# Kernel optimization log

Measured on AMD Instinct MI355X. Metric: run time of the kernel, lower is better.

## Reference

```python
import jax, jax.numpy as jnp
import numpy as np

T, B, L, D = 4, 2, 2048, 4096

def setup_inputs() -> dict:
    key = jax.random.key(0)
    x = jax.random.normal(key, (T, B, L, D), dtype=jnp.float32)
    return {"x": x}

def reference(x):
    # X_t = sum_{s<=t} x_s ; Y_t = silu(X_t) ; out_t = Y_t - Y_{t-1}, Y_{-1}=0
    X = jnp.cumsum(x, axis=0)            # (T,B,L,D)
    Y = jax.nn.silu(X)                   # act_fn default "silu"
    Y_prev = jnp.concatenate([jnp.zeros_like(Y[:1]), Y[:-1]], axis=0)
    return Y - Y_prev
```

## Files before the change

### kernel.cpp

```cpp
#include <hip/hip_runtime.h>
#include <math.h>


#define T_STEPS 4

__global__ __launch_bounds__(256) void ActSWL_kernel(const float* __restrict__ x,
                                                     float* __restrict__ out,
                                                     long long n_inner_vec,
                                                     long long stride_vec) {
    long long i = (long long)blockIdx.x * blockDim.x + threadIdx.x;
    if (i >= n_inner_vec) return;

    const float4* __restrict__ xv = reinterpret_cast<const float4*>(x);
    float4* __restrict__ ov       = reinterpret_cast<float4*>(out);

    float4 X     = make_float4(0.f, 0.f, 0.f, 0.f);
    float4 Yprev = make_float4(0.f, 0.f, 0.f, 0.f);

#pragma unroll
    for (int t = 0; t < T_STEPS; ++t) {
        float4 v = xv[i + (long long)t * stride_vec];

        X.x += v.x; X.y += v.y; X.z += v.z; X.w += v.w;

        float4 Y;
        Y.x = X.x / (1.0f + __expf(-X.x));
        Y.y = X.y / (1.0f + __expf(-X.y));
        Y.z = X.z / (1.0f + __expf(-X.z));
        Y.w = X.w / (1.0f + __expf(-X.w));

        float4 o;
        o.x = Y.x - Yprev.x;
        o.y = Y.y - Yprev.y;
        o.z = Y.z - Yprev.z;
        o.w = Y.w - Yprev.w;

        ov[i + (long long)t * stride_vec] = o;

        Yprev = Y;
    }
}

extern "C" void kernel_launch(void* const* d_in, const int* in_sizes, int n_in,
                              void* d_out, int out_size, void* d_ws, size_t ws_size,
                              hipStream_t stream) {
    const float* x = (const float*)d_in[0];
    float* out     = (float*)d_out;

    const long long n_total   = (long long)in_sizes[0];
    const long long n_inner   = n_total / T_STEPS;
    const long long n_vec     = n_inner / 4;
    const long long stridev   = n_vec;

    const int block = 256;
    const long long grid = (n_vec + block - 1) / block;

    ActSWL_kernel<<<dim3((unsigned)grid), dim3(block), 0, stream>>>(x, out, n_vec, stridev);
}
```

Measured before the change: 435.8 us.

## Use nontemporal vector loads/stores, hoist loads, fast reciprocal, 32-bit indexing

Rewrites the elementwise cumsum-silu-diff kernel so that all four time-step loads are issued up front as nontemporal loads, and outputs are written with nontemporal stores. The division is replaced with a hardware reciprocal builtin, and index math is switched from 64-bit to 32-bit. The aim is more memory-level parallelism, less cache pollution on a streaming, bandwidth-bound kernel, and cheaper address arithmetic. It trades some precision from the approximate reciprocal and relies on the 32-bit indices staying within range for this size.

```diff
diff --git a/kernel.cpp b/kernel.cpp
--- a/kernel.cpp
+++ b/kernel.cpp
@@ -4,56 +4,54 @@
 
 #define T_STEPS 4
 
-__global__ __launch_bounds__(256) void ActSWL_kernel(const float* __restrict__ x,
-                                                     float* __restrict__ out,
-                                                     long long n_inner_vec,
-                                                     long long stride_vec) {
-    long long i = (long long)blockIdx.x * blockDim.x + threadIdx.x;
-    if (i >= n_inner_vec) return;
+typedef float v4f __attribute__((ext_vector_type(4)));
 
-    const float4* __restrict__ xv = reinterpret_cast<const float4*>(x);
-    float4* __restrict__ ov       = reinterpret_cast<float4*>(out);
+__device__ __forceinline__ v4f silu4(v4f X) {
+    v4f r;
+    r.x = X.x * __builtin_amdgcn_rcpf(1.0f + __expf(-X.x));
+    r.y = X.y * __builtin_amdgcn_rcpf(1.0f + __expf(-X.y));
+    r.z = X.z * __builtin_amdgcn_rcpf(1.0f + __expf(-X.z));
+    r.w = X.w * __builtin_amdgcn_rcpf(1.0f + __expf(-X.w));
+    return r;
+}
 
-    float4 X     = make_float4(0.f, 0.f, 0.f, 0.f);
-    float4 Yprev = make_float4(0.f, 0.f, 0.f, 0.f);
+__global__ __launch_bounds__(256) void ActSWL_kernel(const v4f* __restrict__ xv,
+                                                     v4f* __restrict__ ov,
+                                                     unsigned n_vec) {
+    unsigned i = blockIdx.x * 256u + threadIdx.x;
+    if (i >= n_vec) return;
 
-#pragma unroll
-    for (int t = 0; t < T_STEPS; ++t) {
-        float4 v = xv[i + (long long)t * stride_vec];
+    v4f v0 = __builtin_nontemporal_load(xv + i);
+    v4f v1 = __builtin_nontemporal_load(xv + i + n_vec);
+    v4f v2 = __builtin_nontemporal_load(xv + i + 2u * n_vec);
+    v4f v3 = __builtin_nontemporal_load(xv + i + 3u * n_vec);
 
-        X.x += v.x; X.y += v.y; X.z += v.z; X.w += v.w;
+    v4f X  = v0;
+    v4f y0 = silu4(X);
+    X += v1;
+    v4f y1 = silu4(X);
+    X += v2;
+    v4f y2 = silu4(X);
+    X += v3;
+    v4f y3 = silu4(X);
 
-        float4 Y;
-        Y.x = X.x / (1.0f + __expf(-X.x));
-        Y.y = X.y / (1.0f + __expf(-X.y));
-        Y.z = X.z / (1.0f + __expf(-X.z));
-        Y.w = X.w / (1.0f + __expf(-X.w));
-
-        float4 o;
-        o.x = Y.x - Yprev.x;
-        o.y = Y.y - Yprev.y;
-        o.z = Y.z - Yprev.z;
-        o.w = Y.w - Yprev.w;
-
-        ov[i + (long long)t * stride_vec] = o;
-
-        Yprev = Y;
-    }
+    __builtin_nontemporal_store(y0,      ov + i);
+    __builtin_nontemporal_store(y1 - y0, ov + i + n_vec);
+    __builtin_nontemporal_store(y2 - y1, ov + i + 2u * n_vec);
+    __builtin_nontemporal_store(y3 - y2, ov + i + 3u * n_vec);
 }
 
 extern "C" void kernel_launch(void* const* d_in, const int* in_sizes, int n_in,
                               void* d_out, int out_size, void* d_ws, size_t ws_size,
                               hipStream_t stream) {
-    const float* x = (const float*)d_in[0];
-    float* out     = (float*)d_out;
+    const v4f* xv = (const v4f*)d_in[0];
+    v4f* ov       = (v4f*)d_out;
 
-    const long long n_total   = (long long)in_sizes[0];
-    const long long n_inner   = n_total / T_STEPS;
-    const long long n_vec     = n_inner / 4;
-    const long long stridev   = n_vec;
+    const long long n_total = (long long)in_sizes[0];
+    const unsigned n_vec    = (unsigned)(n_total / T_STEPS / 4);
 
     const int block = 256;
-    const long long grid = (n_vec + block - 1) / block;
+    const unsigned grid = (n_vec + block - 1) / block;
 
-    ActSWL_kernel<<<dim3((unsigned)grid), dim3(block), 0, stream>>>(x, out, n_vec, stridev);
+    ActSWL_kernel<<<dim3(grid), dim3(block), 0, stream>>>(xv, ov, n_vec);
 }
```

After: 431.7 us. No clear change (-0.9%).
